# Optimization experiments

Measured on AMD Instinct MI355X. Metric: run time of the kernel, lower is better.

Reference implementation:

```python
import jax, jax.numpy as jnp
import numpy as np

GRID_SIZE = 64
K = 3
GRID_RANGE = (-1.0, 1.0)
NUM_BASIS = GRID_SIZE + K


def _knots():
    # extended knot vector: k repeats of the left end, uniform grid, k repeats of the right end
    g = jnp.linspace(GRID_RANGE[0], GRID_RANGE[1], GRID_SIZE + 1, dtype=jnp.float32)
    left = jnp.full((K,), GRID_RANGE[0], dtype=jnp.float32)
    right = jnp.full((K,), GRID_RANGE[1], dtype=jnp.float32)
    return jnp.concatenate([left, g, right])  # (GRID_SIZE + 2K + 1,)


def reference(x):
    """Cox-de Boor B-spline basis, bottom-up DP (vectorized over batch).

    x: (B,) float32 -> (B, NUM_BASIS) float32
    """
    knots = _knots()
    n0 = GRID_SIZE + 2 * K  # number of degree-0 basis functions
    xb = x[:, None]  # (B, 1)
    # degree 0: indicator of half-open interval [t_i, t_{i+1})
    N = ((xb >= knots[None, :n0]) & (xb < knots[None, 1:n0 + 1])).astype(x.dtype)
    for d in range(1, K + 1):
        n = n0 - d  # number of degree-d bases
        t_i = knots[:n]
        t_id = knots[d:d + n]
        t_i1 = knots[1:1 + n]
        t_id1 = knots[d + 1:d + 1 + n]
        den1 = t_id - t_i
        den2 = t_id1 - t_i1
        # term is dropped entirely when the denominator is zero (repeated knots)
        w1 = jnp.where(den1 != 0, (xb - t_i) / jnp.where(den1 != 0, den1, 1.0), 0.0)
        w2 = jnp.where(den2 != 0, (t_id1 - xb) / jnp.where(den2 != 0, den2, 1.0), 0.0)
        N = w1 * N[:, :n] + w2 * N[:, 1:n + 1]
    return N  # (B, NUM_BASIS)


def setup_inputs() -> dict:
    key = jax.random.key(0)
    x = jax.random.uniform(key, (2_000_000,), minval=-1.0, maxval=1.0, dtype=jnp.float32)
    return {"x": x}
```

## Files before the change

kernel.cpp:

```cpp
#include <hip/hip_runtime.h>

#define ROWS_PER_BLOCK 128
#define NUM_BASIS 67
#define TILE_FLOATS (ROWS_PER_BLOCK * NUM_BASIS)
#define TILE_VEC4 (TILE_FLOATS / 4)

__device__ __forceinline__ float kv(int i) {
    i = min(max(i, 3), 67);
    return (float)(i - 35) * 0.03125f;
}

__global__ __launch_bounds__(256) void SplineBasis_kernel(const float* __restrict__ x,
                                                          float* __restrict__ out,
                                                          int B) {
    __shared__ __align__(16) float tile[TILE_FLOATS];
    const int tid = threadIdx.x;
    const int blockRow0 = blockIdx.x * ROWS_PER_BLOCK;

    float4* t4 = (float4*)tile;
    for (int i = tid; i < TILE_VEC4; i += 256) t4[i] = make_float4(0.f, 0.f, 0.f, 0.f);
    __syncthreads();

    if (tid < ROWS_PER_BLOCK) {
        const int row = blockRow0 + tid;
        if (row < B) {
            const float xv = x[row];
            if (xv >= -1.0f && xv < 1.0f) {
                int cell = (int)floorf((xv + 1.0f) * 32.0f);
                cell = min(max(cell, 0), 63);
                int m = cell + 3;
                while (m > 3 && xv < kv(m)) --m;
                while (m < 66 && xv >= kv(m + 1)) ++m;

                float N[4], left[4], right[4];
                N[0] = 1.0f;
#pragma unroll
                for (int d = 1; d <= 3; ++d) {
                    left[d]  = xv - kv(m + 1 - d);
                    right[d] = kv(m + d) - xv;
                    float saved = 0.0f;
#pragma unroll
                    for (int r = 0; r < d; ++r) {
                        float temp = N[r] / (right[r + 1] + left[d - r]);
                        N[r] = saved + right[r + 1] * temp;
                        saved = left[d - r] * temp;
                    }
                    N[d] = saved;
                }

                const int c0 = tid * NUM_BASIS + (m - 3);
                tile[c0 + 0] = N[0];
                tile[c0 + 1] = N[1];
                tile[c0 + 2] = N[2];
                tile[c0 + 3] = N[3];
            }
        }
    }
    __syncthreads();

    const int rows = min(ROWS_PER_BLOCK, B - blockRow0);
    if (rows == ROWS_PER_BLOCK) {
        float4* o4 = (float4*)(out + (size_t)blockRow0 * NUM_BASIS);
        for (int i = tid; i < TILE_VEC4; i += 256) o4[i] = t4[i];
    } else if (rows > 0) {
        const int n = rows * NUM_BASIS;
        float* o = out + (size_t)blockRow0 * NUM_BASIS;
        for (int i = tid; i < n; i += 256) o[i] = tile[i];
    }
}

extern "C" void kernel_launch(void* const* d_in, const int* in_sizes, int n_in,
                              void* d_out, int out_size, void* d_ws, size_t ws_size,
                              hipStream_t stream) {
    const float* x = (const float*)d_in[0];
    float* out = (float*)d_out;
    const int B = in_sizes[0];
    const int nblocks = (B + ROWS_PER_BLOCK - 1) / ROWS_PER_BLOCK;
    SplineBasis_kernel<<<nblocks, 256, 0, stream>>>(x, out, B);
}
```

Before: 526.2 us.

## Compute basis per output float4 directly, removing shared-memory tile staging

```diff
diff --git a/kernel.cpp b/kernel.cpp
--- a/kernel.cpp
+++ b/kernel.cpp
@@ -1,71 +1,86 @@
 #include <hip/hip_runtime.h>
 
-#define ROWS_PER_BLOCK 128
 #define NUM_BASIS 67
-#define TILE_FLOATS (ROWS_PER_BLOCK * NUM_BASIS)
-#define TILE_VEC4 (TILE_FLOATS / 4)
 
 __device__ __forceinline__ float kv(int i) {
     i = min(max(i, 3), 67);
     return (float)(i - 35) * 0.03125f;
 }
 
-__global__ __launch_bounds__(256) void SplineBasis_kernel(const float* __restrict__ x,
-                                                          float* __restrict__ out,
-                                                          int B) {
-    __shared__ __align__(16) float tile[TILE_FLOATS];
-    const int tid = threadIdx.x;
-    const int blockRow0 = blockIdx.x * ROWS_PER_BLOCK;
+__device__ __forceinline__ void row_basis(float xv, int& m, float N[4]) {
+    N[0] = N[1] = N[2] = N[3] = 0.0f;
+    m = 1 << 20;
+    if (xv >= -1.0f && xv < 1.0f) {
+        int cell = (int)floorf((xv + 1.0f) * 32.0f);
+        cell = min(max(cell, 0), 63);
+        m = cell + 3;
+        while (m > 3 && xv < kv(m)) --m;
+        while (m < 66 && xv >= kv(m + 1)) ++m;
 
-    float4* t4 = (float4*)tile;
-    for (int i = tid; i < TILE_VEC4; i += 256) t4[i] = make_float4(0.f, 0.f, 0.f, 0.f);
-    __syncthreads();
-
-    if (tid < ROWS_PER_BLOCK) {
-        const int row = blockRow0 + tid;
-        if (row < B) {
-            const float xv = x[row];
-            if (xv >= -1.0f && xv < 1.0f) {
-                int cell = (int)floorf((xv + 1.0f) * 32.0f);
-                cell = min(max(cell, 0), 63);
-                int m = cell + 3;
-                while (m > 3 && xv < kv(m)) --m;
-                while (m < 66 && xv >= kv(m + 1)) ++m;
-
-                float N[4], left[4], right[4];
-                N[0] = 1.0f;
+        float left[4], right[4];
+        N[0] = 1.0f;
 #pragma unroll
-                for (int d = 1; d <= 3; ++d) {
-                    left[d]  = xv - kv(m + 1 - d);
-                    right[d] = kv(m + d) - xv;
-                    float saved = 0.0f;
+        for (int d = 1; d <= 3; ++d) {
+            left[d] = xv - kv(m + 1 - d);
+            right[d] = kv(m + d) - xv;
+            float saved = 0.0f;
 #pragma unroll
-                    for (int r = 0; r < d; ++r) {
-                        float temp = N[r] / (right[r + 1] + left[d - r]);
-                        N[r] = saved + right[r + 1] * temp;
-                        saved = left[d - r] * temp;
-                    }
-                    N[d] = saved;
-                }
-
-                const int c0 = tid * NUM_BASIS + (m - 3);
-                tile[c0 + 0] = N[0];
-                tile[c0 + 1] = N[1];
-                tile[c0 + 2] = N[2];
-                tile[c0 + 3] = N[3];
+            for (int r = 0; r < d; ++r) {
+                float temp = __fdividef(N[r], right[r + 1] + left[d - r]);
+                N[r] = saved + right[r + 1] * temp;
+                saved = left[d - r] * temp;
             }
+            N[d] = saved;
         }
     }
-    __syncthreads();
+}
 
-    const int rows = min(ROWS_PER_BLOCK, B - blockRow0);
-    if (rows == ROWS_PER_BLOCK) {
-        float4* o4 = (float4*)(out + (size_t)blockRow0 * NUM_BASIS);
-        for (int i = tid; i < TILE_VEC4; i += 256) o4[i] = t4[i];
-    } else if (rows > 0) {
-        const int n = rows * NUM_BASIS;
-        float* o = out + (size_t)blockRow0 * NUM_BASIS;
-        for (int i = tid; i < n; i += 256) o[i] = tile[i];
+__device__ __forceinline__ float sel(int c, int m, const float N[4]) {
+    const int d = c - (m - 3);
+    float v = 0.0f;
+    v = (d == 0) ? N[0] : v;
+    v = (d == 1) ? N[1] : v;
+    v = (d == 2) ? N[2] : v;
+    v = (d == 3) ? N[3] : v;
+    return v;
+}
+
+__global__ __launch_bounds__(256) void SplineBasis_kernel(const float* __restrict__ x,
+                                                          float4* __restrict__ out4,
+                                                          int n4, int out_size, int B) {
+    const int g4 = blockIdx.x * 256 + threadIdx.x;
+    if (g4 < n4) {
+        const int g = g4 * 4;
+        const int row0 = g / NUM_BASIS;
+        const int col0 = g - row0 * NUM_BASIS;
+
+        int m0;
+        float N0[4];
+        row_basis(x[row0], m0, N0);
+
+        int m1 = 1 << 20;
+        float N1[4] = {0.f, 0.f, 0.f, 0.f};
+        if (col0 > NUM_BASIS - 4 && row0 + 1 < B) {
+            row_basis(x[row0 + 1], m1, N1);
+        }
+
+        float4 v;
+        int c;
+        c = col0 + 0; v.x = (c < NUM_BASIS) ? sel(c, m0, N0) : sel(c - NUM_BASIS, m1, N1);
+        c = col0 + 1; v.y = (c < NUM_BASIS) ? sel(c, m0, N0) : sel(c - NUM_BASIS, m1, N1);
+        c = col0 + 2; v.z = (c < NUM_BASIS) ? sel(c, m0, N0) : sel(c - NUM_BASIS, m1, N1);
+        c = col0 + 3; v.w = (c < NUM_BASIS) ? sel(c, m0, N0) : sel(c - NUM_BASIS, m1, N1);
+        out4[g4] = v;
+    } else if (g4 == n4) {
+        float* out = (float*)out4;
+        for (int g = n4 * 4; g < out_size; ++g) {
+            const int row = g / NUM_BASIS;
+            const int col = g - row * NUM_BASIS;
+            int m;
+            float N[4];
+            row_basis(x[row], m, N);
+            out[g] = sel(col, m, N);
+        }
     }
 }
 
@@ -73,8 +88,9 @@
                               void* d_out, int out_size, void* d_ws, size_t ws_size,
                               hipStream_t stream) {
     const float* x = (const float*)d_in[0];
-    float* out = (float*)d_out;
     const int B = in_sizes[0];
-    const int nblocks = (B + ROWS_PER_BLOCK - 1) / ROWS_PER_BLOCK;
-    SplineBasis_kernel<<<nblocks, 256, 0, stream>>>(x, out, B);
+    const int n4 = out_size / 4;
+    const int nthreads = n4 + ((out_size & 3) ? 1 : 0);
+    const int nblocks = (nthreads + 255) / 256;
+    SplineBasis_kernel<<<nblocks, 256, 0, stream>>>(x, (float4*)d_out, n4, out_size, B);
 }
```

Result: slower. 933.9 us (+77.5%).

## Store compact per-row span in LDS and synthesize dense output on store

Applied to the files above, without the earlier changes.

```diff
diff --git a/kernel.cpp b/kernel.cpp
--- a/kernel.cpp
+++ b/kernel.cpp
@@ -1,7 +1,7 @@
 #include <hip/hip_runtime.h>
 
+#define NUM_BASIS 67
 #define ROWS_PER_BLOCK 128
-#define NUM_BASIS 67
 #define TILE_FLOATS (ROWS_PER_BLOCK * NUM_BASIS)
 #define TILE_VEC4 (TILE_FLOATS / 4)
 
@@ -10,62 +10,89 @@
     return (float)(i - 35) * 0.03125f;
 }
 
+__device__ __forceinline__ void row_basis(float xv, int& m, float N[4]) {
+    N[0] = N[1] = N[2] = N[3] = 0.0f;
+    m = 1 << 20;
+    if (xv >= -1.0f && xv < 1.0f) {
+        int cell = (int)floorf((xv + 1.0f) * 32.0f);
+        cell = min(max(cell, 0), 63);
+        m = cell + 3;
+        while (m > 3 && xv < kv(m)) --m;
+        while (m < 66 && xv >= kv(m + 1)) ++m;
+
+        float left[4], right[4];
+        N[0] = 1.0f;
+#pragma unroll
+        for (int d = 1; d <= 3; ++d) {
+            left[d] = xv - kv(m + 1 - d);
+            right[d] = kv(m + d) - xv;
+            float saved = 0.0f;
+#pragma unroll
+            for (int r = 0; r < d; ++r) {
+                float temp = N[r] / (right[r + 1] + left[d - r]);
+                N[r] = saved + right[r + 1] * temp;
+                saved = left[d - r] * temp;
+            }
+            N[d] = saved;
+        }
+    }
+}
+
+__device__ __forceinline__ float pick(int d, float4 n) {
+    float v = 0.0f;
+    v = (d == 0) ? n.x : v;
+    v = (d == 1) ? n.y : v;
+    v = (d == 2) ? n.z : v;
+    v = (d == 3) ? n.w : v;
+    return v;
+}
+
 __global__ __launch_bounds__(256) void SplineBasis_kernel(const float* __restrict__ x,
                                                           float* __restrict__ out,
                                                           int B) {
-    __shared__ __align__(16) float tile[TILE_FLOATS];
+    __shared__ int s_m[ROWS_PER_BLOCK];
+    __shared__ float4 s_N[ROWS_PER_BLOCK];
     const int tid = threadIdx.x;
     const int blockRow0 = blockIdx.x * ROWS_PER_BLOCK;
 
-    float4* t4 = (float4*)tile;
-    for (int i = tid; i < TILE_VEC4; i += 256) t4[i] = make_float4(0.f, 0.f, 0.f, 0.f);
-    __syncthreads();
-
     if (tid < ROWS_PER_BLOCK) {
+        int m = 1 << 20;
+        float N[4] = {0.f, 0.f, 0.f, 0.f};
         const int row = blockRow0 + tid;
-        if (row < B) {
-            const float xv = x[row];
-            if (xv >= -1.0f && xv < 1.0f) {
-                int cell = (int)floorf((xv + 1.0f) * 32.0f);
-                cell = min(max(cell, 0), 63);
-                int m = cell + 3;
-                while (m > 3 && xv < kv(m)) --m;
-                while (m < 66 && xv >= kv(m + 1)) ++m;
-
-                float N[4], left[4], right[4];
-                N[0] = 1.0f;
-#pragma unroll
-                for (int d = 1; d <= 3; ++d) {
-                    left[d]  = xv - kv(m + 1 - d);
-                    right[d] = kv(m + d) - xv;
-                    float saved = 0.0f;
-#pragma unroll
-                    for (int r = 0; r < d; ++r) {
-                        float temp = N[r] / (right[r + 1] + left[d - r]);
-                        N[r] = saved + right[r + 1] * temp;
-                        saved = left[d - r] * temp;
-                    }
-                    N[d] = saved;
-                }
-
-                const int c0 = tid * NUM_BASIS + (m - 3);
-                tile[c0 + 0] = N[0];
-                tile[c0 + 1] = N[1];
-                tile[c0 + 2] = N[2];
-                tile[c0 + 3] = N[3];
-            }
-        }
+        if (row < B) row_basis(x[row], m, N);
+        s_m[tid] = m;
+        s_N[tid] = make_float4(N[0], N[1], N[2], N[3]);
     }
     __syncthreads();
 
     const int rows = min(ROWS_PER_BLOCK, B - blockRow0);
     if (rows == ROWS_PER_BLOCK) {
         float4* o4 = (float4*)(out + (size_t)blockRow0 * NUM_BASIS);
-        for (int i = tid; i < TILE_VEC4; i += 256) o4[i] = t4[i];
+        for (int i = tid; i < TILE_VEC4; i += 256) {
+            const int g = i * 4;
+            const int r0 = (int)((unsigned)g / NUM_BASIS);
+            const int c0 = g - r0 * NUM_BASIS;
+            const int r1 = min(r0 + 1, ROWS_PER_BLOCK - 1);
+            const int m0 = s_m[r0];
+            const int m1 = s_m[r1];
+            const float4 n0 = s_N[r0];
+            const float4 n1 = s_N[r1];
+            float4 v;
+            int c;
+            c = c0 + 0; v.x = (c < NUM_BASIS) ? pick(c - m0 + 3, n0) : pick(c - NUM_BASIS - m1 + 3, n1);
+            c = c0 + 1; v.y = (c < NUM_BASIS) ? pick(c - m0 + 3, n0) : pick(c - NUM_BASIS - m1 + 3, n1);
+            c = c0 + 2; v.z = (c < NUM_BASIS) ? pick(c - m0 + 3, n0) : pick(c - NUM_BASIS - m1 + 3, n1);
+            c = c0 + 3; v.w = (c < NUM_BASIS) ? pick(c - m0 + 3, n0) : pick(c - NUM_BASIS - m1 + 3, n1);
+            o4[i] = v;
+        }
     } else if (rows > 0) {
         const int n = rows * NUM_BASIS;
         float* o = out + (size_t)blockRow0 * NUM_BASIS;
-        for (int i = tid; i < n; i += 256) o[i] = tile[i];
+        for (int i = tid; i < n; i += 256) {
+            const int r0 = (int)((unsigned)i / NUM_BASIS);
+            const int c0 = i - r0 * NUM_BASIS;
+            o[i] = pick(c0 - s_m[r0] + 3, s_N[r0]);
+        }
     }
 }
 
```

After: 533.3 us. No clear change (+1.4%).
